# Optimization experiments

Hardware: AMD Instinct MI355X
Metric: run time of the kernel (lower is better)

The kernel has to match this reference:

```python
import jax, jax.numpy as jnp
import numpy as np

D_CONV = 4  # matches Mamba(d_conv=4)


def _silu(v):
    return v * jax.nn.sigmoid(v)


def _mamba_block(x, in_w, cw, cb, xw, dtw, dtb, A_log, Dp, ow):
    # x: (B, L, d_model)
    B, L, _ = x.shape
    d_inner, d_state = A_log.shape
    xz = x @ in_w.T                        # (B, L, 2*d_inner)
    xr, z = jnp.split(xz, 2, axis=-1)      # each (B, L, d_inner)
    # causal depthwise conv1d (pad d_conv-1 on the left, truncate to L)
    xp = jnp.pad(xr, ((0, 0), (D_CONV - 1, 0), (0, 0)))
    xc = sum(xp[:, k:k + L, :] * cw[:, k] for k in range(D_CONV)) + cb
    xc = _silu(xc)                         # (B, L, d_inner)
    dbl = xc @ xw.T                        # (B, L, dt_rank + 2*d_state)
    dt_rank = dbl.shape[-1] - 2 * d_state
    dt, Bm, Cm = jnp.split(dbl, [dt_rank, dt_rank + d_state], axis=-1)
    dt = jax.nn.softplus(dt @ dtw.T + dtb)  # (B, L, d_inner)
    A = -jnp.exp(A_log)                    # (d_inner, d_state)
    dA = jnp.exp(dt[..., None] * A)                          # (B, L, d_inner, d_state)
    dBx = dt[..., None] * Bm[:, :, None, :] * xc[..., None]  # (B, L, d_inner, d_state)

    def step(h, inputs):
        dA_t, dBx_t, C_t = inputs          # (B,d,s), (B,d,s), (B,s)
        h = dA_t * h + dBx_t
        y = jnp.einsum('bds,bs->bd', h, C_t)
        return h, y

    h0 = jnp.zeros((B, d_inner, d_state), x.dtype)
    _, ys = jax.lax.scan(step, h0, (dA.transpose(1, 0, 2, 3),
                                    dBx.transpose(1, 0, 2, 3),
                                    Cm.transpose(1, 0, 2)))
    y = ys.transpose(1, 0, 2) + xc * Dp    # skip term D*u
    y = y * _silu(z)                       # gated
    return y @ ow.T                        # (B, L, d_model)


def setup_inputs() -> dict:
    key = jax.random.key(0)
    d_model, d_state, n_layer = 1024, 16, 2
    d_inner = 2 * d_model
    dt_rank = d_model // 16  # ceil(1024/16)
    Bsz, L = 2, 1024
    ks = jax.random.split(key, 8)
    s = 0.02
    x = jax.random.normal(ks[0], (Bsz, L, d_model), jnp.float32)
    in_proj_w = jax.random.normal(ks[1], (n_layer, 2 * d_inner, d_model), jnp.float32) * s
    conv_w = jax.random.normal(ks[2], (n_layer, d_inner, D_CONV), jnp.float32) * 0.2
    conv_b = jnp.zeros((n_layer, d_inner), jnp.float32)
    x_proj_w = jax.random.normal(ks[3], (n_layer, dt_rank + 2 * d_state, d_inner), jnp.float32) * s
    dt_proj_w = jax.random.normal(ks[4], (n_layer, d_inner, dt_rank), jnp.float32) * s
    dt_proj_b = jax.random.uniform(ks[5], (n_layer, d_inner), jnp.float32, -5.0, -3.0)
    A_log = jnp.log(jnp.tile(jnp.arange(1, d_state + 1, dtype=jnp.float32), (n_layer, d_inner, 1)))
    D = jnp.ones((n_layer, d_inner), jnp.float32)
    out_proj_w = jax.random.normal(ks[6], (n_layer, d_model, d_inner), jnp.float32) * s
    return {"x": x, "in_proj_w": in_proj_w, "conv_w": conv_w, "conv_b": conv_b,
            "x_proj_w": x_proj_w, "dt_proj_w": dt_proj_w, "dt_proj_b": dt_proj_b,
            "A_log": A_log, "D": D, "out_proj_w": out_proj_w}


def reference(x, in_proj_w, conv_w, conv_b, x_proj_w, dt_proj_w, dt_proj_b, A_log, D, out_proj_w):
    n_layer = in_proj_w.shape[0]
    for i in range(n_layer):
        x = _mamba_block(x, in_proj_w[i], conv_w[i], conv_b[i], x_proj_w[i],
                         dt_proj_w[i], dt_proj_b[i], A_log[i], D[i], out_proj_w[i])
    return x
```

## Files before the change

### kernel.cpp

```cpp
#include <hip/hip_runtime.h>
#include <hip/hip_bf16.h>
#include <cmath>

typedef __bf16 bf16x8_t __attribute__((ext_vector_type(8)));
typedef float  f32x4_t  __attribute__((ext_vector_type(4)));
using bf16 = __hip_bfloat16;

#define LOG2E 1.44269504088896340736f
#define LN2   0.69314718055994530942f

#define AS1C(p) ((const __attribute__((address_space(1))) void*)(p))
#define AS3C(p) ((__attribute__((address_space(3))) void*)(p))

__device__ __forceinline__ float fexp2(float x) { return __builtin_amdgcn_exp2f(x); }
__device__ __forceinline__ float flog2(float x) { return __builtin_amdgcn_logf(x); }
__device__ __forceinline__ float frcp (float x) { return __builtin_amdgcn_rcpf(x); }

__global__ __launch_bounds__(256)
void cast_multi(const float* s0, bf16* d0, int e0,
                const float* s1, bf16* d1, int e1,
                const float* s2, bf16* d2, int e2,
                const float* s3, bf16* d3, int e3,
                const float* s4, bf16* d4, int e4)
{
    const int blk = blockIdx.x;
    const float* src; bf16* dst; int base;
    if      (blk < e0) { src = s0; dst = d0; base = blk; }
    else if (blk < e1) { src = s1; dst = d1; base = blk - e0; }
    else if (blk < e2) { src = s2; dst = d2; base = blk - e1; }
    else if (blk < e3) { src = s3; dst = d3; base = blk - e2; }
    else               { src = s4; dst = d4; base = blk - e3; }

    const int i = base * 256 + threadIdx.x;
    const float4* s = (const float4*)(src + (size_t)i * 8);
    float4 a = s[0], b = s[1];
    bf16 o[8];
    o[0] = __float2bfloat16(a.x); o[1] = __float2bfloat16(a.y);
    o[2] = __float2bfloat16(a.z); o[3] = __float2bfloat16(a.w);
    o[4] = __float2bfloat16(b.x); o[5] = __float2bfloat16(b.y);
    o[6] = __float2bfloat16(b.z); o[7] = __float2bfloat16(b.w);
    *(int4*)(dst + (size_t)i * 8) = *(int4*)o;
}

template<int MODE, bool SPLITK>
__global__ __launch_bounds__(256)
void gemm_bf16(const bf16* __restrict__ A, const bf16* __restrict__ B,
               float* __restrict__ Cf, bf16* __restrict__ Cb,
               int M, int N, int K, int lda, int ldb, int ldc)
{
    __shared__ __align__(16) bf16 At[2][128][32];
    __shared__ __align__(16) bf16 Bt[2][128][32];

    const int tid  = threadIdx.x;
    const int lane = tid & 63;
    const int wid  = tid >> 6;
    const int wr   = wid >> 1;
    const int wc   = wid & 1;
    const int fr   = lane & 15;
    const int fq   = lane >> 4;

    const int row0 = blockIdx.y * 128;
    const int col0 = blockIdx.x * 128;
    const int kb   = SPLITK ? blockIdx.z * K : 0;

    const int g_row = wid * 32 + (lane >> 2);
    const int g_kp  = (((lane & 3) ^ ((lane >> 3) & 3)) * 8);
    const bf16* aP0 = A + (size_t)(row0 + g_row) * lda + g_kp + kb;
    const bf16* aP1 = A + (size_t)(row0 + g_row + 16) * lda + g_kp + kb;
    int bR0 = col0 + g_row;      if (bR0 >= N) bR0 = N - 1;
    int bR1 = col0 + g_row + 16; if (bR1 >= N) bR1 = N - 1;
    const bf16* bP0 = B + (size_t)bR0 * ldb + g_kp + kb;
    const bf16* bP1 = B + (size_t)bR1 * ldb + g_kp + kb;

    const int rchunk = (fq ^ ((fr >> 1) & 3)) * 8;

    f32x4_t acc[4][4];
    #pragma unroll
    for (int m = 0; m < 4; ++m)
        #pragma unroll
        for (int n = 0; n < 4; ++n)
            acc[m][n] = f32x4_t{0.f, 0.f, 0.f, 0.f};

    auto STAGE = [&](int buf, int k0) {
        __builtin_amdgcn_global_load_lds(AS1C(aP0 + k0), AS3C(&At[buf][wid * 32][0]),      16, 0, 0);
        __builtin_amdgcn_global_load_lds(AS1C(aP1 + k0), AS3C(&At[buf][wid * 32 + 16][0]), 16, 0, 0);
        __builtin_amdgcn_global_load_lds(AS1C(bP0 + k0), AS3C(&Bt[buf][wid * 32][0]),      16, 0, 0);
        __builtin_amdgcn_global_load_lds(AS1C(bP1 + k0), AS3C(&Bt[buf][wid * 32 + 16][0]), 16, 0, 0);
    };

    STAGE(0, 0);
    __syncthreads();
    int cur = 0;
    for (int k0 = 0; k0 < K; k0 += 32) {
        if (k0 + 32 < K) STAGE(cur ^ 1, k0 + 32);

        bf16x8_t af[4], bg[4];
        #pragma unroll
        for (int m = 0; m < 4; ++m)
            af[m] = *(const bf16x8_t*)&At[cur][wr * 64 + m * 16 + fr][rchunk];
        #pragma unroll
        for (int n = 0; n < 4; ++n)
            bg[n] = *(const bf16x8_t*)&Bt[cur][wc * 64 + n * 16 + fr][rchunk];
        #pragma unroll
        for (int m = 0; m < 4; ++m)
            #pragma unroll
            for (int n = 0; n < 4; ++n)
                acc[m][n] = __builtin_amdgcn_mfma_f32_16x16x32_bf16(
                    af[m], bg[n], acc[m][n], 0, 0, 0);

        __syncthreads();
        cur ^= 1;
    }

    float* Cfz = SPLITK ? (Cf + (size_t)blockIdx.z * M * ldc) : Cf;

    #pragma unroll
    for (int m = 0; m < 4; ++m) {
        #pragma unroll
        for (int n = 0; n < 4; ++n) {
            const int c = col0 + wc * 64 + n * 16 + fr;
            if (c < N) {
                #pragma unroll
                for (int r = 0; r < 4; ++r) {
                    const int rr = row0 + wr * 64 + m * 16 + fq * 4 + r;
                    if (SPLITK || MODE != 1) Cfz[(size_t)rr * ldc + c] = acc[m][n][r];
                    if (!SPLITK && MODE != 0) Cb[(size_t)rr * ldc + c] = __float2bfloat16(acc[m][n][r]);
                }
            }
        }
    }
}

__global__ __launch_bounds__(256)
void reduce_pk(const float* __restrict__ part, float* __restrict__ of,
               bf16* __restrict__ oh, int n4, int stride4, int S)
{
    const int i = blockIdx.x * blockDim.x + threadIdx.x;
    if (i >= n4) return;
    const float4* p4 = (const float4*)part;
    float4 s = p4[i];
    for (int k = 1; k < S; ++k) {
        float4 v = p4[(size_t)k * stride4 + i];
        s.x += v.x; s.y += v.y; s.z += v.z; s.w += v.w;
    }
    if (of) ((float4*)of)[i] = s;
    if (oh) {
        bf16 o[4];
        o[0] = __float2bfloat16(s.x); o[1] = __float2bfloat16(s.y);
        o[2] = __float2bfloat16(s.z); o[3] = __float2bfloat16(s.w);
        *(int2*)(oh + (size_t)i * 4) = *(int2*)o;
    }
}

__global__ __launch_bounds__(256)
void conv_silu(const bf16* __restrict__ xz, const float* __restrict__ cw,
               const float* __restrict__ cb, bf16* __restrict__ xc,
               int Bsz, int L, int dinner)
{
    const int nv = dinner / 4;
    const int g  = blockIdx.x * blockDim.x + threadIdx.x;
    const int d4 = (g % nv) * 4;
    const int t  = (g / nv) % L;
    const int b  = g / (nv * L);
    if (b >= Bsz) return;

    const int ldxz = 2 * dinner;
    float4 w0 = *(const float4*)(cw + (size_t)(d4 + 0) * 4);
    float4 w1 = *(const float4*)(cw + (size_t)(d4 + 1) * 4);
    float4 w2 = *(const float4*)(cw + (size_t)(d4 + 2) * 4);
    float4 w3 = *(const float4*)(cw + (size_t)(d4 + 3) * 4);
    float4 acc = *(const float4*)(cb + d4);

    const bf16* base = xz + (size_t)b * L * ldxz + d4;
    #pragma unroll
    for (int k = 0; k < 4; ++k) {
        const int ts = t - 3 + k;
        if (ts >= 0) {
            const bf16* rp = base + (size_t)ts * ldxz;
            float vx = __bfloat162float(rp[0]);
            float vy = __bfloat162float(rp[1]);
            float vz = __bfloat162float(rp[2]);
            float vw = __bfloat162float(rp[3]);
            acc.x = fmaf(vx, (&w0.x)[k], acc.x);
            acc.y = fmaf(vy, (&w1.x)[k], acc.y);
            acc.z = fmaf(vz, (&w2.x)[k], acc.z);
            acc.w = fmaf(vw, (&w3.x)[k], acc.w);
        }
    }
    acc.x = acc.x * frcp(1.f + fexp2(-acc.x * LOG2E));
    acc.y = acc.y * frcp(1.f + fexp2(-acc.y * LOG2E));
    acc.z = acc.z * frcp(1.f + fexp2(-acc.z * LOG2E));
    acc.w = acc.w * frcp(1.f + fexp2(-acc.w * LOG2E));

    bf16 o[4];
    o[0] = __float2bfloat16(acc.x); o[1] = __float2bfloat16(acc.y);
    o[2] = __float2bfloat16(acc.z); o[3] = __float2bfloat16(acc.w);
    *(int2*)(xc + ((size_t)b * L + t) * dinner + d4) = *(int2*)o;
}

__global__ __launch_bounds__(256)
void scan_part1(const bf16* __restrict__ dtraw, const bf16* __restrict__ xc,
                const float* __restrict__ dbl, const float* __restrict__ dtb,
                const float* __restrict__ alog, float* __restrict__ hend,
                float* __restrict__ Ssum, int Bsz, int L, int dinner,
                int NC, int CL)
{
    const int g = blockIdx.x * blockDim.x + threadIdx.x;
    const int d = g % dinner;
    const int c = (g / dinner) % NC;
    const int b = g / (dinner * NC);
    if (b >= Bsz) return;

    const float* ap = alog + (size_t)d * 16;
    float a_[16];
    *(float4*)&a_[0]  = *(const float4*)(ap + 0);
    *(float4*)&a_[4]  = *(const float4*)(ap + 4);
    *(float4*)&a_[8]  = *(const float4*)(ap + 8);
    *(float4*)&a_[12] = *(const float4*)(ap + 12);
    float As[16];
    #pragma unroll
    for (int i = 0; i < 16; ++i) As[i] = -fexp2(a_[i] * LOG2E) * LOG2E;
    const float bias = dtb[d];

    const int t0 = c * CL;
    const bf16*  dt_p = dtraw + ((size_t)b * L + t0) * dinner + d;
    const bf16*  xc_p = xc    + ((size_t)b * L + t0) * dinner + d;
    const float* bl_p = dbl   + ((size_t)b * L + t0) * 96 + 64;

    float h[16];
    #pragma unroll
    for (int i = 0; i < 16; ++i) h[i] = 0.f;
    float S = 0.f;

    for (int t = 0; t < CL; ++t) {
        const float dtv = __bfloat162float(*dt_p);
        const float xcv = __bfloat162float(*xc_p);
        float Bv[16];
        *(float4*)&Bv[0]  = *(const float4*)(bl_p + 0);
        *(float4*)&Bv[4]  = *(const float4*)(bl_p + 4);
        *(float4*)&Bv[8]  = *(const float4*)(bl_p + 8);
        *(float4*)&Bv[12] = *(const float4*)(bl_p + 12);

        const float xv = dtv + bias;
        const float e  = fexp2(xv * LOG2E);
        const float sp = (xv > 15.f) ? xv : LN2 * flog2(1.f + e);
        S += sp;
        const float u = sp * xcv;
        #pragma unroll
        for (int i = 0; i < 16; ++i)
            h[i] = fmaf(fexp2(sp * As[i]), h[i], u * Bv[i]);

        dt_p += dinner; xc_p += dinner; bl_p += 96;
    }

    const size_t idx = ((size_t)b * NC + c) * dinner + d;
    float* hp = hend + idx * 16;
    *(float4*)(hp + 0)  = make_float4(h[0],  h[1],  h[2],  h[3]);
    *(float4*)(hp + 4)  = make_float4(h[4],  h[5],  h[6],  h[7]);
    *(float4*)(hp + 8)  = make_float4(h[8],  h[9],  h[10], h[11]);
    *(float4*)(hp + 12) = make_float4(h[12], h[13], h[14], h[15]);
    Ssum[idx] = S;
}

__global__ __launch_bounds__(256)
void chunk_prefix(float* __restrict__ hend, const float* __restrict__ Ssum,
                  const float* __restrict__ alog, int Bsz, int dinner, int NC)
{
    const int g = blockIdx.x * blockDim.x + threadIdx.x;
    const int s = g & 15;
    const int d = (g >> 4) % dinner;
    const int b = g / (16 * dinner);
    if (b >= Bsz) return;

    const float As2 = -fexp2(alog[(size_t)d * 16 + s] * LOG2E) * LOG2E;

    float h = 0.f;
    for (int c = 0; c < NC; ++c) {
        const size_t idx = ((size_t)b * NC + c) * dinner + d;
        const float he = hend[idx * 16 + s];
        const float Sv = Ssum[idx];
        hend[idx * 16 + s] = h;
        h = fmaf(fexp2(As2 * Sv), h, he);
    }
}

__global__ __launch_bounds__(256)
void scan_part2(bf16* dty, const bf16* __restrict__ xc,
                const float* __restrict__ dbl, const bf16* __restrict__ xz,
                const float* __restrict__ dtb, const float* __restrict__ alog,
                const float* __restrict__ Dp, const float* __restrict__ hinit,
                int Bsz, int L, int dinner, int NC, int CL)
{
    const int g = blockIdx.x * blockDim.x + threadIdx.x;
    const int d = g % dinner;
    const int c = (g / dinner) % NC;
    const int b = g / (dinner * NC);
    if (b >= Bsz) return;

    const float* ap = alog + (size_t)d * 16;
    float a_[16];
    *(float4*)&a_[0]  = *(const float4*)(ap + 0);
    *(float4*)&a_[4]  = *(const float4*)(ap + 4);
    *(float4*)&a_[8]  = *(const float4*)(ap + 8);
    *(float4*)&a_[12] = *(const float4*)(ap + 12);
    float As[16];
    #pragma unroll
    for (int i = 0; i < 16; ++i) As[i] = -fexp2(a_[i] * LOG2E) * LOG2E;
    const float bias = dtb[d];
    const float Dval = Dp[d];

    const size_t cidx = ((size_t)b * NC + c) * dinner + d;
    float h[16];
    const float* hp = hinit + cidx * 16;
    *(float4*)&h[0]  = *(const float4*)(hp + 0);
    *(float4*)&h[4]  = *(const float4*)(hp + 4);
    *(float4*)&h[8]  = *(const float4*)(hp + 8);
    *(float4*)&h[12] = *(const float4*)(hp + 12);

    const int t0 = c * CL;
    bf16*        dt_p = dty + ((size_t)b * L + t0) * dinner + d;
    const bf16*  xc_p = xc  + ((size_t)b * L + t0) * dinner + d;
    const float* bl_p = dbl + ((size_t)b * L + t0) * 96 + 64;
    const bf16*  z_p  = xz  + ((size_t)b * L + t0) * (2 * dinner) + dinner + d;

    for (int t = 0; t < CL; ++t) {
        const float dtv = __bfloat162float(*dt_p);
        const float xcv = __bfloat162float(*xc_p);
        const float zv  = __bfloat162float(*z_p);
        float Bv[16], Cv[16];
        *(float4*)&Bv[0]  = *(const float4*)(bl_p + 0);
        *(float4*)&Bv[4]  = *(const float4*)(bl_p + 4);
        *(float4*)&Bv[8]  = *(const float4*)(bl_p + 8);
        *(float4*)&Bv[12] = *(const float4*)(bl_p + 12);
        *(float4*)&Cv[0]  = *(const float4*)(bl_p + 16);
        *(float4*)&Cv[4]  = *(const float4*)(bl_p + 20);
        *(float4*)&Cv[8]  = *(const float4*)(bl_p + 24);
        *(float4*)&Cv[12] = *(const float4*)(bl_p + 28);

        const float xv = dtv + bias;
        const float e  = fexp2(xv * LOG2E);
        const float sp = (xv > 15.f) ? xv : LN2 * flog2(1.f + e);
        const float u = sp * xcv;
        float y = 0.f;
        #pragma unroll
        for (int i = 0; i < 16; ++i) {
            h[i] = fmaf(fexp2(sp * As[i]), h[i], u * Bv[i]);
            y = fmaf(h[i], Cv[i], y);
        }

        y = fmaf(xcv, Dval, y);
        const float sig = frcp(1.f + fexp2(-zv * LOG2E));
        *dt_p = __float2bfloat16(y * (zv * sig));

        dt_p += dinner; xc_p += dinner; bl_p += 96; z_p += 2 * dinner;
    }
}

extern "C" void kernel_launch(void* const* d_in, const int* in_sizes, int n_in,
                              void* d_out, int out_size, void* d_ws, size_t ws_size,
                              hipStream_t stream)
{
    const float* x    = (const float*)d_in[0];
    const float* inw  = (const float*)d_in[1];
    const float* cw   = (const float*)d_in[2];
    const float* cb   = (const float*)d_in[3];
    const float* xw   = (const float*)d_in[4];
    const float* dtw  = (const float*)d_in[5];
    const float* dtb  = (const float*)d_in[6];
    const float* alog = (const float*)d_in[7];
    const float* Dp   = (const float*)d_in[8];
    const float* ow   = (const float*)d_in[9];
    float* out = (float*)d_out;

    const int Bsz = 2, L = 1024, dmodel = 1024, dinner = 2048;
    const int BL = Bsz * L;
    const int NC = 64, CL = L / NC;
    const int SPX = 16, KSX = dinner / SPX;
    const int SPO = 2,  KSO = dinner / SPO;

    char* p = (char*)d_ws;
    auto alloc = [&](size_t bytes) { char* r = p; p += (bytes + 63) & ~size_t(63); return r; };
    bf16*  wb_in  = (bf16*) alloc((size_t)2 * 2 * dinner * dmodel * 2);
    bf16*  wb_x   = (bf16*) alloc((size_t)2 * 96 * dinner * 2);
    bf16*  wb_dt  = (bf16*) alloc((size_t)2 * dinner * 64 * 2);
    bf16*  wb_ow  = (bf16*) alloc((size_t)2 * dmodel * dinner * 2);
    bf16*  curb   = (bf16*) alloc((size_t)BL * dmodel * 2);
    bf16*  xzb16  = (bf16*) alloc((size_t)BL * 2 * dinner * 2);
    bf16*  xcb16  = (bf16*) alloc((size_t)BL * dinner * 2);
    float* dblb   = (float*)alloc((size_t)BL * 96 * 4);
    bf16*  dblb16 = (bf16*) alloc((size_t)BL * 96 * 2);
    bf16*  dtrb16 = (bf16*) alloc((size_t)BL * dinner * 2);
    float* ssumb  = (float*)alloc((size_t)Bsz * NC * dinner * 4);
    float* partb  = (float*)alloc((size_t)SPO * BL * dmodel * 4);
    float* hendb  = partb;

    const int scan_blocks = (Bsz * NC * dinner) / 256;
    const int pfx_blocks  = (Bsz * dinner * 16) / 256;

    {
        const int n8_x  = BL * dmodel / 8;
        const int n8_in = 2 * 2 * dinner * dmodel / 8;
        const int n8_xw = 2 * 96 * dinner / 8;
        const int n8_dt = 2 * dinner * 64 / 8;
        const int n8_ow = 2 * dmodel * dinner / 8;
        const int e0 = n8_x / 256;
        const int e1 = e0 + n8_in / 256;
        const int e2 = e1 + n8_xw / 256;
        const int e3 = e2 + n8_dt / 256;
        const int e4 = e3 + n8_ow / 256;
        cast_multi<<<e4, 256, 0, stream>>>(
            x, curb, e0, inw, wb_in, e1, xw, wb_x, e2, dtw, wb_dt, e3, ow, wb_ow, e4);
    }

    for (int l = 0; l < 2; ++l) {
        const bf16*  wb_in_l = wb_in + (size_t)l * 2 * dinner * dmodel;
        const bf16*  wb_x_l  = wb_x  + (size_t)l * 96 * dinner;
        const bf16*  wb_dt_l = wb_dt + (size_t)l * dinner * 64;
        const bf16*  wb_ow_l = wb_ow + (size_t)l * dmodel * dinner;
        const float* cw_l    = cw   + (size_t)l * dinner * 4;
        const float* cb_l    = cb   + (size_t)l * dinner;
        const float* dtb_l   = dtb  + (size_t)l * dinner;
        const float* alog_l  = alog + (size_t)l * dinner * 16;
        const float* Dp_l    = Dp   + (size_t)l * dinner;

        gemm_bf16<1, false><<<dim3(2 * dinner / 128, BL / 128), 256, 0, stream>>>(
            curb, wb_in_l, nullptr, xzb16, BL, 2 * dinner, dmodel, dmodel, dmodel, 2 * dinner);

        conv_silu<<<(BL * dinner / 4) / 256, 256, 0, stream>>>(
            xzb16, cw_l, cb_l, xcb16, Bsz, L, dinner);

        gemm_bf16<0, true><<<dim3(1, BL / 128, SPX), 256, 0, stream>>>(
            xcb16, wb_x_l, partb, nullptr, BL, 96, KSX, dinner, dinner, 96);
        reduce_pk<<<(BL * 96 / 4 + 255) / 256, 256, 0, stream>>>(
            partb, dblb, dblb16, BL * 96 / 4, BL * 96 / 4, SPX);

        gemm_bf16<1, false><<<dim3(dinner / 128, BL / 128), 256, 0, stream>>>(
            dblb16, wb_dt_l, nullptr, dtrb16, BL, dinner, 64, 96, 64, dinner);

        scan_part1<<<scan_blocks, 256, 0, stream>>>(
            dtrb16, xcb16, dblb, dtb_l, alog_l, hendb, ssumb, Bsz, L, dinner, NC, CL);
        chunk_prefix<<<pfx_blocks, 256, 0, stream>>>(
            hendb, ssumb, alog_l, Bsz, dinner, NC);
        scan_part2<<<scan_blocks, 256, 0, stream>>>(
            dtrb16, xcb16, dblb, xzb16, dtb_l, alog_l, Dp_l, hendb,
            Bsz, L, dinner, NC, CL);

        gemm_bf16<0, true><<<dim3(dmodel / 128, BL / 128, SPO), 256, 0, stream>>>(
            dtrb16, wb_ow_l, partb, nullptr, BL, dmodel, KSO, dinner, dinner, dmodel);
        if (l == 0)
            reduce_pk<<<(BL * dmodel / 4 + 255) / 256, 256, 0, stream>>>(
                partb, nullptr, curb, BL * dmodel / 4, BL * dmodel / 4, SPO);
        else
            reduce_pk<<<(BL * dmodel / 4 + 255) / 256, 256, 0, stream>>>(
                partb, out, nullptr, BL * dmodel / 4, BL * dmodel / 4, SPO);
    }
}
```

Baseline: 333.9 us.

## Shrink GEMM M-tile to 64, register-block conv over time, tune scan chunks

The GEMM tile shrinks from 128x128 to 64x128, so each wave computes a 32x64 sub-tile and the grid doubles, giving more blocks across the CUs. The conv+SiLU kernel now has each thread produce four consecutive timesteps from seven loaded rows, reusing overlapping input instead of reloading it. The chunk-prefix loop prefetches the next chunk's values, and the scan chunk count drops from 64 to 32. Together these trade per-block MFMA reuse for parallelism and cut redundant loads, but smaller tiles raise the global-to-LDS traffic per FLOP.

```diff
diff --git a/kernel.cpp b/kernel.cpp
--- a/kernel.cpp
+++ b/kernel.cpp
@@ -48,42 +48,41 @@
                float* __restrict__ Cf, bf16* __restrict__ Cb,
                int M, int N, int K, int lda, int ldb, int ldc)
 {
-    __shared__ __align__(16) bf16 At[2][128][32];
+    __shared__ __align__(16) bf16 At[2][64][32];
     __shared__ __align__(16) bf16 Bt[2][128][32];
 
     const int tid  = threadIdx.x;
     const int lane = tid & 63;
     const int wid  = tid >> 6;
-    const int wr   = wid >> 1;
-    const int wc   = wid & 1;
+    const int wr2  = wid & 1;
+    const int wc2  = wid >> 1;
     const int fr   = lane & 15;
     const int fq   = lane >> 4;
 
-    const int row0 = blockIdx.y * 128;
+    const int row0 = blockIdx.y * 64;
     const int col0 = blockIdx.x * 128;
     const int kb   = SPLITK ? blockIdx.z * K : 0;
 
-    const int g_row = wid * 32 + (lane >> 2);
-    const int g_kp  = (((lane & 3) ^ ((lane >> 3) & 3)) * 8);
-    const bf16* aP0 = A + (size_t)(row0 + g_row) * lda + g_kp + kb;
-    const bf16* aP1 = A + (size_t)(row0 + g_row + 16) * lda + g_kp + kb;
-    int bR0 = col0 + g_row;      if (bR0 >= N) bR0 = N - 1;
-    int bR1 = col0 + g_row + 16; if (bR1 >= N) bR1 = N - 1;
+    const int gA_row = wid * 16 + (lane >> 2);
+    const int gB_row = wid * 32 + (lane >> 2);
+    const int g_kp   = (((lane & 3) ^ ((lane >> 3) & 3)) * 8);
+    const bf16* aP0 = A + (size_t)(row0 + gA_row) * lda + g_kp + kb;
+    int bR0 = col0 + gB_row;      if (bR0 >= N) bR0 = N - 1;
+    int bR1 = col0 + gB_row + 16; if (bR1 >= N) bR1 = N - 1;
     const bf16* bP0 = B + (size_t)bR0 * ldb + g_kp + kb;
     const bf16* bP1 = B + (size_t)bR1 * ldb + g_kp + kb;
 
     const int rchunk = (fq ^ ((fr >> 1) & 3)) * 8;
 
-    f32x4_t acc[4][4];
-    #pragma unroll
-    for (int m = 0; m < 4; ++m)
+    f32x4_t acc[2][4];
+    #pragma unroll
+    for (int m = 0; m < 2; ++m)
         #pragma unroll
         for (int n = 0; n < 4; ++n)
             acc[m][n] = f32x4_t{0.f, 0.f, 0.f, 0.f};
 
     auto STAGE = [&](int buf, int k0) {
-        __builtin_amdgcn_global_load_lds(AS1C(aP0 + k0), AS3C(&At[buf][wid * 32][0]),      16, 0, 0);
-        __builtin_amdgcn_global_load_lds(AS1C(aP1 + k0), AS3C(&At[buf][wid * 32 + 16][0]), 16, 0, 0);
+        __builtin_amdgcn_global_load_lds(AS1C(aP0 + k0), AS3C(&At[buf][wid * 16][0]),      16, 0, 0);
         __builtin_amdgcn_global_load_lds(AS1C(bP0 + k0), AS3C(&Bt[buf][wid * 32][0]),      16, 0, 0);
         __builtin_amdgcn_global_load_lds(AS1C(bP1 + k0), AS3C(&Bt[buf][wid * 32 + 16][0]), 16, 0, 0);
     };
@@ -94,15 +93,15 @@
     for (int k0 = 0; k0 < K; k0 += 32) {
         if (k0 + 32 < K) STAGE(cur ^ 1, k0 + 32);
 
-        bf16x8_t af[4], bg[4];
-        #pragma unroll
-        for (int m = 0; m < 4; ++m)
-            af[m] = *(const bf16x8_t*)&At[cur][wr * 64 + m * 16 + fr][rchunk];
+        bf16x8_t af[2], bg[4];
+        #pragma unroll
+        for (int m = 0; m < 2; ++m)
+            af[m] = *(const bf16x8_t*)&At[cur][wr2 * 32 + m * 16 + fr][rchunk];
         #pragma unroll
         for (int n = 0; n < 4; ++n)
-            bg[n] = *(const bf16x8_t*)&Bt[cur][wc * 64 + n * 16 + fr][rchunk];
-        #pragma unroll
-        for (int m = 0; m < 4; ++m)
+            bg[n] = *(const bf16x8_t*)&Bt[cur][wc2 * 64 + n * 16 + fr][rchunk];
+        #pragma unroll
+        for (int m = 0; m < 2; ++m)
             #pragma unroll
             for (int n = 0; n < 4; ++n)
                 acc[m][n] = __builtin_amdgcn_mfma_f32_16x16x32_bf16(
@@ -115,14 +114,14 @@
     float* Cfz = SPLITK ? (Cf + (size_t)blockIdx.z * M * ldc) : Cf;
 
     #pragma unroll
-    for (int m = 0; m < 4; ++m) {
+    for (int m = 0; m < 2; ++m) {
         #pragma unroll
         for (int n = 0; n < 4; ++n) {
-            const int c = col0 + wc * 64 + n * 16 + fr;
+            const int c = col0 + wc2 * 64 + n * 16 + fr;
             if (c < N) {
                 #pragma unroll
                 for (int r = 0; r < 4; ++r) {
-                    const int rr = row0 + wr * 64 + m * 16 + fq * 4 + r;
+                    const int rr = row0 + wr2 * 32 + m * 16 + fq * 4 + r;
                     if (SPLITK || MODE != 1) Cfz[(size_t)rr * ldc + c] = acc[m][n][r];
                     if (!SPLITK && MODE != 0) Cb[(size_t)rr * ldc + c] = __float2bfloat16(acc[m][n][r]);
                 }
@@ -158,44 +157,57 @@
                int Bsz, int L, int dinner)
 {
     const int nv = dinner / 4;
+    const int L4 = L / 4;
     const int g  = blockIdx.x * blockDim.x + threadIdx.x;
     const int d4 = (g % nv) * 4;
-    const int t  = (g / nv) % L;
-    const int b  = g / (nv * L);
+    const int t4 = (g / nv) % L4;
+    const int b  = g / (nv * L4);
     if (b >= Bsz) return;
 
+    const int t0 = t4 * 4;
     const int ldxz = 2 * dinner;
+
     float4 w0 = *(const float4*)(cw + (size_t)(d4 + 0) * 4);
     float4 w1 = *(const float4*)(cw + (size_t)(d4 + 1) * 4);
     float4 w2 = *(const float4*)(cw + (size_t)(d4 + 2) * 4);
     float4 w3 = *(const float4*)(cw + (size_t)(d4 + 3) * 4);
-    float4 acc = *(const float4*)(cb + d4);
-
+    float4 bias = *(const float4*)(cb + d4);
+
+    float4 r[7];
     const bf16* base = xz + (size_t)b * L * ldxz + d4;
     #pragma unroll
-    for (int k = 0; k < 4; ++k) {
-        const int ts = t - 3 + k;
-        if (ts >= 0) {
+    for (int k = 0; k < 7; ++k) {
+        const int ts = t0 - 3 + k;
+        if (ts >= 0 && ts < L) {
             const bf16* rp = base + (size_t)ts * ldxz;
-            float vx = __bfloat162float(rp[0]);
-            float vy = __bfloat162float(rp[1]);
-            float vz = __bfloat162float(rp[2]);
-            float vw = __bfloat162float(rp[3]);
-            acc.x = fmaf(vx, (&w0.x)[k], acc.x);
-            acc.y = fmaf(vy, (&w1.x)[k], acc.y);
-            acc.z = fmaf(vz, (&w2.x)[k], acc.z);
-            acc.w = fmaf(vw, (&w3.x)[k], acc.w);
+            r[k] = make_float4(__bfloat162float(rp[0]), __bfloat162float(rp[1]),
+                               __bfloat162float(rp[2]), __bfloat162float(rp[3]));
+        } else {
+            r[k] = make_float4(0.f, 0.f, 0.f, 0.f);
         }
     }
-    acc.x = acc.x * frcp(1.f + fexp2(-acc.x * LOG2E));
-    acc.y = acc.y * frcp(1.f + fexp2(-acc.y * LOG2E));
-    acc.z = acc.z * frcp(1.f + fexp2(-acc.z * LOG2E));
-    acc.w = acc.w * frcp(1.f + fexp2(-acc.w * LOG2E));
-
-    bf16 o[4];
-    o[0] = __float2bfloat16(acc.x); o[1] = __float2bfloat16(acc.y);
-    o[2] = __float2bfloat16(acc.z); o[3] = __float2bfloat16(acc.w);
-    *(int2*)(xc + ((size_t)b * L + t) * dinner + d4) = *(int2*)o;
+
+    bf16* outp = xc + ((size_t)b * L + t0) * dinner + d4;
+    #pragma unroll
+    for (int j = 0; j < 4; ++j) {
+        float4 acc = bias;
+        #pragma unroll
+        for (int k = 0; k < 4; ++k) {
+            const float4 v = r[j + k];
+            acc.x = fmaf(v.x, (&w0.x)[k], acc.x);
+            acc.y = fmaf(v.y, (&w1.x)[k], acc.y);
+            acc.z = fmaf(v.z, (&w2.x)[k], acc.z);
+            acc.w = fmaf(v.w, (&w3.x)[k], acc.w);
+        }
+        acc.x = acc.x * frcp(1.f + fexp2(-acc.x * LOG2E));
+        acc.y = acc.y * frcp(1.f + fexp2(-acc.y * LOG2E));
+        acc.z = acc.z * frcp(1.f + fexp2(-acc.z * LOG2E));
+        acc.w = acc.w * frcp(1.f + fexp2(-acc.w * LOG2E));
+        bf16 o[4];
+        o[0] = __float2bfloat16(acc.x); o[1] = __float2bfloat16(acc.y);
+        o[2] = __float2bfloat16(acc.z); o[3] = __float2bfloat16(acc.w);
+        *(int2*)(outp + (size_t)j * dinner) = *(int2*)o;
+    }
 }
 
 __global__ __launch_bounds__(256)
@@ -274,13 +286,19 @@
 
     const float As2 = -fexp2(alog[(size_t)d * 16 + s] * LOG2E) * LOG2E;
 
+    size_t idx = (size_t)b * NC * dinner + d;
+    float he = hend[idx * 16 + s];
+    float Sv = Ssum[idx];
     float h = 0.f;
     for (int c = 0; c < NC; ++c) {
-        const size_t idx = ((size_t)b * NC + c) * dinner + d;
-        const float he = hend[idx * 16 + s];
-        const float Sv = Ssum[idx];
+        float heN = 0.f, SvN = 0.f;
+        if (c + 1 < NC) {
+            heN = hend[(idx + dinner) * 16 + s];
+            SvN = Ssum[idx + dinner];
+        }
         hend[idx * 16 + s] = h;
         h = fmaf(fexp2(As2 * Sv), h, he);
+        he = heN; Sv = SvN; idx += dinner;
     }
 }
 
@@ -374,7 +392,7 @@
 
     const int Bsz = 2, L = 1024, dmodel = 1024, dinner = 2048;
     const int BL = Bsz * L;
-    const int NC = 64, CL = L / NC;
+    const int NC = 32, CL = L / NC;
     const int SPX = 16, KSX = dinner / SPX;
     const int SPO = 2,  KSO = dinner / SPO;
 
@@ -423,18 +441,18 @@
         const float* alog_l  = alog + (size_t)l * dinner * 16;
         const float* Dp_l    = Dp   + (size_t)l * dinner;
 
-        gemm_bf16<1, false><<<dim3(2 * dinner / 128, BL / 128), 256, 0, stream>>>(
+        gemm_bf16<1, false><<<dim3(2 * dinner / 128, BL / 64), 256, 0, stream>>>(
             curb, wb_in_l, nullptr, xzb16, BL, 2 * dinner, dmodel, dmodel, dmodel, 2 * dinner);
 
-        conv_silu<<<(BL * dinner / 4) / 256, 256, 0, stream>>>(
+        conv_silu<<<(Bsz * (L / 4) * (dinner / 4)) / 256, 256, 0, stream>>>(
             xzb16, cw_l, cb_l, xcb16, Bsz, L, dinner);
 
-        gemm_bf16<0, true><<<dim3(1, BL / 128, SPX), 256, 0, stream>>>(
+        gemm_bf16<0, true><<<dim3(1, BL / 64, SPX), 256, 0, stream>>>(
             xcb16, wb_x_l, partb, nullptr, BL, 96, KSX, dinner, dinner, 96);
         reduce_pk<<<(BL * 96 / 4 + 255) / 256, 256, 0, stream>>>(
             partb, dblb, dblb16, BL * 96 / 4, BL * 96 / 4, SPX);
 
-        gemm_bf16<1, false><<<dim3(dinner / 128, BL / 128), 256, 0, stream>>>(
+        gemm_bf16<1, false><<<dim3(dinner / 128, BL / 64), 256, 0, stream>>>(
             dblb16, wb_dt_l, nullptr, dtrb16, BL, dinner, 64, 96, 64, dinner);
 
         scan_part1<<<scan_blocks, 256, 0, stream>>>(
@@ -445,7 +463,7 @@
             dtrb16, xcb16, dblb, xzb16, dtb_l, alog_l, Dp_l, hendb,
             Bsz, L, dinner, NC, CL);
 
-        gemm_bf16<0, true><<<dim3(dmodel / 128, BL / 128, SPO), 256, 0, stream>>>(
+        gemm_bf16<0, true><<<dim3(dmodel / 128, BL / 64, SPO), 256, 0, stream>>>(
             dtrb16, wb_ow_l, partb, nullptr, BL, dmodel, KSO, dinner, dinner, dmodel);
         if (l == 0)
             reduce_pk<<<(BL * dmodel / 4 + 255) / 256, 256, 0, stream>>>(
```

Result: faster. 319.9 us (-4.2%).
